# Kernel tuning notes

Measured on AMD Instinct MI355X. Metric: run time of the kernel, lower is better.

## Reference

```python
import jax, jax.numpy as jnp
import numpy as np

D_MODEL = 1024
EXPERT_SIZE = 512
N_EXPERTS = 8
GROUP_SIZE = 32
BATCH = 32
SEQ = 2048
TEMPERATURE = 1.0


def setup_inputs() -> dict:
    key = jax.random.key(0)
    k_x, k_l1, k_l2, k_c = jax.random.split(key, 4)
    x = jax.random.normal(k_x, (BATCH, SEQ, D_MODEL), dtype=jnp.float32)
    # truncated-normal-style init approximated with normal scaled by 1/sqrt(fan_in)
    lin1 = jax.random.normal(k_l1, (N_EXPERTS, D_MODEL, EXPERT_SIZE), dtype=jnp.float32) * (D_MODEL ** -0.5)
    lin2 = jax.random.normal(k_l2, (N_EXPERTS, EXPERT_SIZE, D_MODEL), dtype=jnp.float32) * (EXPERT_SIZE ** -0.5)
    controller = jax.random.normal(k_c, (D_MODEL, N_EXPERTS), dtype=jnp.float32) * (D_MODEL ** -0.5)
    return {"x": x, "lin1": lin1, "lin2": lin2, "controller": controller}


def reference(x, lin1, lin2, controller):
    B, S, D = x.shape
    # group_tokens: sparsity_dim=0 -> transpose to (S, B, D), split batch into groups
    xg = jnp.transpose(x, (1, 0, 2)).reshape(S, B // GROUP_SIZE, GROUP_SIZE, D)  # (s, g, k, d)
    # controller logits, softmax over the group (token) axis k (dim=-2)
    logits = jnp.einsum("sgkd,de->sgke", xg, controller) / TEMPERATURE
    merge_w = jax.nn.softmax(logits, axis=-2)  # (s, g, k, e)
    emit_w = merge_w  # default: emit softmax over tokens, same temp -> reuse
    # merge: weighted sum of tokens per expert
    merged = jnp.einsum("sgke,sgkd->sged", merge_w, xg)  # (s, g, e, d)
    # per-expert MLP
    h = jax.nn.relu(jnp.einsum("sged,edf->sgef", merged, lin1))  # (s, g, e, f)
    expert_out = jnp.einsum("sgef,efd->sged", h, lin2)  # (s, g, e, d)
    # emit back to tokens
    out = jnp.einsum("sgke,sged->sgkd", emit_w, expert_out)  # (s, g, k, d)
    # redistribute: (S, B, D) -> (B, S, D)
    return jnp.transpose(out.reshape(S, B, D), (1, 0, 2))
```

## Files before the change

### kernel.cpp

```cpp
#include <hip/hip_runtime.h>
#include <hip/hip_bf16.h>

#define SS 2048
#define BB 32
#define DD 1024
#define FF 512
#define EE 8

typedef __attribute__((ext_vector_type(8))) short short8;
typedef __attribute__((ext_vector_type(8))) unsigned short ushort8v;
typedef __attribute__((ext_vector_type(4))) float f32x4;

__device__ inline unsigned short f2bf(float f) {
  union { float f; unsigned u; } v; v.f = f;
  return (unsigned short)((v.u + 0x7FFFu + ((v.u >> 16) & 1u)) >> 16);
}
__device__ inline float bf2f(unsigned short h) {
  union { unsigned u; float f; } v; v.u = ((unsigned)h) << 16;
  return v.f;
}

__global__ __launch_bounds__(256) void transpose_bf16(
    const float* __restrict__ in, unsigned short* __restrict__ out, int K, int N) {
  __shared__ float tile[32][33];
  int e = blockIdx.z;
  const float* inp = in + (size_t)e * K * N;
  unsigned short* outp = out + (size_t)e * K * N;
  int k0 = blockIdx.x * 32, n0 = blockIdx.y * 32;
  int tx = threadIdx.x;
  int ty = threadIdx.y;
#pragma unroll
  for (int i = 0; i < 4; i++) {
    int k = ty + i * 8;
    tile[k][tx] = inp[(size_t)(k0 + k) * N + n0 + tx];
  }
  __syncthreads();
#pragma unroll
  for (int i = 0; i < 4; i++) {
    int n = ty + i * 8;
    outp[(size_t)(n0 + n) * K + k0 + tx] = f2bf(tile[tx][n]);
  }
}

__global__ __launch_bounds__(256) void ctrl_merge(
    const float* __restrict__ x,
    const float* __restrict__ ctrl,
    unsigned short* __restrict__ merged,
    float* __restrict__ mw) {
  int s = blockIdx.x;
  int t = threadIdx.x;
  __shared__ float cs[DD * EE];
  __shared__ float lg[BB][EE];
  for (int i = t; i < DD * EE; i += 256) cs[i] = ctrl[i];
  __syncthreads();

  int k = t >> 3, e = t & 7;
  const float* xr = x + ((size_t)k * SS + s) * DD;
  float acc = 0.f;
  for (int d = 0; d < DD; d += 4) {
    float4 xv = *(const float4*)&xr[d];
    acc += xv.x * cs[d * 8 + e] + xv.y * cs[(d + 1) * 8 + e] +
           xv.z * cs[(d + 2) * 8 + e] + xv.w * cs[(d + 3) * 8 + e];
  }
  lg[k][e] = acc;
  __syncthreads();

  if (t < EE) {
    float m = -1e30f;
    for (int kk = 0; kk < BB; kk++) m = fmaxf(m, lg[kk][t]);
    float sum = 0.f;
    for (int kk = 0; kk < BB; kk++) sum += __expf(lg[kk][t] - m);
    float inv = 1.f / sum;
    for (int kk = 0; kk < BB; kk++) {
      float w = __expf(lg[kk][t] - m) * inv;
      lg[kk][t] = w;
      mw[((size_t)s * BB + kk) * EE + t] = w;
    }
  }
  __syncthreads();

  float accm[EE][4];
#pragma unroll
  for (int ee = 0; ee < EE; ee++)
#pragma unroll
    for (int j = 0; j < 4; j++) accm[ee][j] = 0.f;
  for (int kk = 0; kk < BB; kk++) {
    float w0 = lg[kk][0], w1 = lg[kk][1], w2 = lg[kk][2], w3 = lg[kk][3];
    float w4 = lg[kk][4], w5 = lg[kk][5], w6 = lg[kk][6], w7 = lg[kk][7];
#pragma unroll
    for (int j = 0; j < 4; j++) {
      float xv = x[((size_t)kk * SS + s) * DD + j * 256 + t];
      accm[0][j] += w0 * xv; accm[1][j] += w1 * xv;
      accm[2][j] += w2 * xv; accm[3][j] += w3 * xv;
      accm[4][j] += w4 * xv; accm[5][j] += w5 * xv;
      accm[6][j] += w6 * xv; accm[7][j] += w7 * xv;
    }
  }
#pragma unroll
  for (int ee = 0; ee < EE; ee++)
#pragma unroll
    for (int j = 0; j < 4; j++)
      merged[((size_t)s * EE + ee) * DD + j * 256 + t] = f2bf(accm[ee][j]);
}

template <int RELU>
__global__ __launch_bounds__(256) void gemm_bt(
    const unsigned short* __restrict__ A, const unsigned short* __restrict__ Bt,
    unsigned short* __restrict__ C, int K, int N) {
  int e = blockIdx.z;
  int m0 = blockIdx.x * 128;
  int n0 = blockIdx.y * 128;
  const int lda = EE * K;
  const unsigned short* Ae = A + (size_t)e * K;
  const unsigned short* Be = Bt + (size_t)e * N * K;

  __shared__ __align__(16) unsigned short As[128][40];
  __shared__ __align__(16) unsigned short Bs[128][40];

  int t = threadIdx.x;
  int lane = t & 63, w = t >> 6;
  int wm = w >> 1, wn = w & 1;
  int lr = lane & 15;
  int kh = lane >> 4;

  f32x4 acc[4][4] = {};

  for (int kt = 0; kt < K; kt += 32) {
#pragma unroll
    for (int i = 0; i < 2; i++) {
      int o = t + i * 256;
      int r = o >> 2, c8 = (o & 3) * 8;
      ushort8v va = *(const ushort8v*)&Ae[(size_t)(m0 + r) * lda + kt + c8];
      *(ushort8v*)&As[r][c8] = va;
      ushort8v vb = *(const ushort8v*)&Be[(size_t)(n0 + r) * K + kt + c8];
      *(ushort8v*)&Bs[r][c8] = vb;
    }
    __syncthreads();

    short8 af[4], bfr[4];
#pragma unroll
    for (int mi = 0; mi < 4; mi++)
      af[mi] = *(const short8*)&As[wm * 64 + mi * 16 + lr][kh * 8];
#pragma unroll
    for (int ni = 0; ni < 4; ni++)
      bfr[ni] = *(const short8*)&Bs[wn * 64 + ni * 16 + lr][kh * 8];
#pragma unroll
    for (int mi = 0; mi < 4; mi++)
#pragma unroll
      for (int ni = 0; ni < 4; ni++)
        acc[mi][ni] = __builtin_amdgcn_mfma_f32_16x16x32_bf16(af[mi], bfr[ni], acc[mi][ni], 0, 0, 0);
    __syncthreads();
  }

  int rb = (lane >> 4) * 4;
  int cb = lane & 15;
#pragma unroll
  for (int mi = 0; mi < 4; mi++)
#pragma unroll
    for (int ni = 0; ni < 4; ni++)
#pragma unroll
      for (int r = 0; r < 4; r++) {
        float v = acc[mi][ni][r];
        if (RELU) v = fmaxf(v, 0.f);
        int m = m0 + wm * 64 + mi * 16 + rb + r;
        int n = n0 + wn * 64 + ni * 16 + cb;
        C[(size_t)m * (EE * N) + (size_t)e * N + n] = f2bf(v);
      }
}

__global__ __launch_bounds__(256) void emit_out(
    const unsigned short* __restrict__ eo,
    const float* __restrict__ mw,
    float* __restrict__ out) {
  int s = blockIdx.x;
  int t = threadIdx.x;
  __shared__ float w[BB][EE];
  w[t >> 3][t & 7] = mw[(size_t)s * BB * EE + t];
  __syncthreads();
  float ev[EE][4];
#pragma unroll
  for (int ee = 0; ee < EE; ee++)
#pragma unroll
    for (int j = 0; j < 4; j++)
      ev[ee][j] = bf2f(eo[((size_t)s * EE + ee) * DD + j * 256 + t]);
  for (int b = 0; b < BB; b++) {
#pragma unroll
    for (int j = 0; j < 4; j++) {
      float acc = 0.f;
#pragma unroll
      for (int ee = 0; ee < EE; ee++) acc += w[b][ee] * ev[ee][j];
      out[((size_t)b * SS + s) * DD + j * 256 + t] = acc;
    }
  }
}

extern "C" void kernel_launch(void* const* d_in, const int* in_sizes, int n_in,
                              void* d_out, int out_size, void* d_ws, size_t ws_size,
                              hipStream_t stream) {
  const float* x = (const float*)d_in[0];
  const float* lin1 = (const float*)d_in[1];
  const float* lin2 = (const float*)d_in[2];
  const float* ctrl = (const float*)d_in[3];
  float* out = (float*)d_out;

  char* ws = (char*)d_ws;
  size_t off = 0;
  unsigned short* lin1t = (unsigned short*)(ws + off); off += (size_t)EE * DD * FF * 2;
  unsigned short* lin2t = (unsigned short*)(ws + off); off += (size_t)EE * FF * DD * 2;
  unsigned short* merged = (unsigned short*)(ws + off); off += (size_t)SS * EE * DD * 2;
  unsigned short* hbuf = (unsigned short*)(ws + off); off += (size_t)SS * EE * FF * 2;
  unsigned short* eo = (unsigned short*)(ws + off); off += (size_t)SS * EE * DD * 2;
  float* mw = (float*)(ws + off); off += (size_t)SS * BB * EE * 4;

  dim3 tb(32, 8);
  transpose_bf16<<<dim3(DD / 32, FF / 32, EE), tb, 0, stream>>>(lin1, lin1t, DD, FF);
  transpose_bf16<<<dim3(FF / 32, DD / 32, EE), tb, 0, stream>>>(lin2, lin2t, FF, DD);

  ctrl_merge<<<SS, 256, 0, stream>>>(x, ctrl, merged, mw);

  gemm_bt<1><<<dim3(SS / 128, FF / 128, EE), 256, 0, stream>>>(merged, lin1t, hbuf, DD, FF);
  gemm_bt<0><<<dim3(SS / 128, DD / 128, EE), 256, 0, stream>>>(hbuf, lin2t, eo, FF, DD);

  emit_out<<<SS, 256, 0, stream>>>(eo, mw, out);
}
```

Measured before the change: 317.4 us.

## Restructure controller-merge kernel with LDS-staged x and coalesced vector I/O

Rewrites ctrl_merge to use 512 threads and read each x row once with coalesced float4 loads. It stages a bf16 copy of the 32 tokens in LDS for the merge pass instead of rereading x from global memory. Logits are reduced with wave shuffles, and the softmax runs in parallel across lanes. emit_out switches to 4-wide bf16 loads and float4 stores. The cost is bf16 rounding of x before the merge, a small accuracy change, plus about 80KB of LDS per block, which limits occupancy.

```diff
diff --git a/kernel.cpp b/kernel.cpp
--- a/kernel.cpp
+++ b/kernel.cpp
@@ -9,6 +9,7 @@
 
 typedef __attribute__((ext_vector_type(8))) short short8;
 typedef __attribute__((ext_vector_type(8))) unsigned short ushort8v;
+typedef __attribute__((ext_vector_type(4))) unsigned short ushort4v;
 typedef __attribute__((ext_vector_type(4))) float f32x4;
 
 __device__ inline unsigned short f2bf(float f) {
@@ -42,65 +43,110 @@
   }
 }
 
-__global__ __launch_bounds__(256) void ctrl_merge(
+__global__ __launch_bounds__(512) void ctrl_merge(
     const float* __restrict__ x,
     const float* __restrict__ ctrl,
     unsigned short* __restrict__ merged,
     float* __restrict__ mw) {
   int s = blockIdx.x;
   int t = threadIdx.x;
-  __shared__ float cs[DD * EE];
-  __shared__ float lg[BB][EE];
-  for (int i = t; i < DD * EE; i += 256) cs[i] = ctrl[i];
-  __syncthreads();
-
-  int k = t >> 3, e = t & 7;
-  const float* xr = x + ((size_t)k * SS + s) * DD;
-  float acc = 0.f;
-  for (int d = 0; d < DD; d += 4) {
-    float4 xv = *(const float4*)&xr[d];
-    acc += xv.x * cs[d * 8 + e] + xv.y * cs[(d + 1) * 8 + e] +
-           xv.z * cs[(d + 2) * 8 + e] + xv.w * cs[(d + 3) * 8 + e];
-  }
-  lg[k][e] = acc;
-  __syncthreads();
-
-  if (t < EE) {
-    float m = -1e30f;
-    for (int kk = 0; kk < BB; kk++) m = fmaxf(m, lg[kk][t]);
-    float sum = 0.f;
-    for (int kk = 0; kk < BB; kk++) sum += __expf(lg[kk][t] - m);
-    float inv = 1.f / sum;
-    for (int kk = 0; kk < BB; kk++) {
-      float w = __expf(lg[kk][t] - m) * inv;
-      lg[kk][t] = w;
-      mw[((size_t)s * BB + kk) * EE + t] = w;
+  int lane = t & 63, w = t >> 6;
+
+  __shared__ float cs[EE][DD];
+  __shared__ unsigned short xs[BB][DD];
+  __shared__ float wl[BB][EE];
+
+  for (int i = t; i < DD * EE; i += 512) {
+    int e2 = i >> 10, d = i & 1023;
+    cs[e2][d] = ctrl[(size_t)d * EE + e2];
+  }
+  __syncthreads();
+
+  float acc[4][8] = {};
+#pragma unroll
+  for (int i = 0; i < 4; i++) {
+    int dbase = lane * 4 + i * 256;
+    float4 c4[8];
+#pragma unroll
+    for (int e2 = 0; e2 < 8; e2++) c4[e2] = *(const float4*)&cs[e2][dbase];
+#pragma unroll
+    for (int kk = 0; kk < 4; kk++) {
+      int k = (w << 2) + kk;
+      float4 xv = *(const float4*)&x[((size_t)k * SS + s) * DD + dbase];
+      ushort4v pv;
+      pv[0] = f2bf(xv.x); pv[1] = f2bf(xv.y); pv[2] = f2bf(xv.z); pv[3] = f2bf(xv.w);
+      *(ushort4v*)&xs[k][dbase] = pv;
+#pragma unroll
+      for (int e2 = 0; e2 < 8; e2++)
+        acc[kk][e2] += xv.x * c4[e2].x + xv.y * c4[e2].y + xv.z * c4[e2].z + xv.w * c4[e2].w;
     }
   }
-  __syncthreads();
-
-  float accm[EE][4];
-#pragma unroll
-  for (int ee = 0; ee < EE; ee++)
-#pragma unroll
-    for (int j = 0; j < 4; j++) accm[ee][j] = 0.f;
-  for (int kk = 0; kk < BB; kk++) {
-    float w0 = lg[kk][0], w1 = lg[kk][1], w2 = lg[kk][2], w3 = lg[kk][3];
-    float w4 = lg[kk][4], w5 = lg[kk][5], w6 = lg[kk][6], w7 = lg[kk][7];
-#pragma unroll
-    for (int j = 0; j < 4; j++) {
-      float xv = x[((size_t)kk * SS + s) * DD + j * 256 + t];
-      accm[0][j] += w0 * xv; accm[1][j] += w1 * xv;
-      accm[2][j] += w2 * xv; accm[3][j] += w3 * xv;
-      accm[4][j] += w4 * xv; accm[5][j] += w5 * xv;
-      accm[6][j] += w6 * xv; accm[7][j] += w7 * xv;
-    }
-  }
-#pragma unroll
-  for (int ee = 0; ee < EE; ee++)
-#pragma unroll
-    for (int j = 0; j < 4; j++)
-      merged[((size_t)s * EE + ee) * DD + j * 256 + t] = f2bf(accm[ee][j]);
+#pragma unroll
+  for (int off = 1; off < 64; off <<= 1)
+#pragma unroll
+    for (int kk = 0; kk < 4; kk++)
+#pragma unroll
+      for (int e2 = 0; e2 < 8; e2++)
+        acc[kk][e2] += __shfl_xor(acc[kk][e2], off, 64);
+  if (lane == 0) {
+#pragma unroll
+    for (int kk = 0; kk < 4; kk++)
+#pragma unroll
+      for (int e2 = 0; e2 < 8; e2++)
+        wl[(w << 2) + kk][e2] = acc[kk][e2];
+  }
+  __syncthreads();
+
+  if (t < 32) {
+    float lgv[8], mx[8], p[8], sm[8];
+#pragma unroll
+    for (int e2 = 0; e2 < 8; e2++) { lgv[e2] = wl[t][e2]; mx[e2] = lgv[e2]; }
+#pragma unroll
+    for (int off = 1; off < 32; off <<= 1)
+#pragma unroll
+      for (int e2 = 0; e2 < 8; e2++)
+        mx[e2] = fmaxf(mx[e2], __shfl_xor(mx[e2], off, 64));
+#pragma unroll
+    for (int e2 = 0; e2 < 8; e2++) { p[e2] = __expf(lgv[e2] - mx[e2]); sm[e2] = p[e2]; }
+#pragma unroll
+    for (int off = 1; off < 32; off <<= 1)
+#pragma unroll
+      for (int e2 = 0; e2 < 8; e2++)
+        sm[e2] += __shfl_xor(sm[e2], off, 64);
+    float wv[8];
+#pragma unroll
+    for (int e2 = 0; e2 < 8; e2++) { wv[e2] = p[e2] / sm[e2]; wl[t][e2] = wv[e2]; }
+    float4 mv0 = {wv[0], wv[1], wv[2], wv[3]};
+    float4 mv1 = {wv[4], wv[5], wv[6], wv[7]};
+    float* mwp = &mw[((size_t)s * BB + t) * EE];
+    *(float4*)mwp = mv0;
+    *(float4*)(mwp + 4) = mv1;
+  }
+  __syncthreads();
+
+  int d0 = t << 1;
+  float a0[8] = {}, a1[8] = {};
+#pragma unroll 4
+  for (int k = 0; k < 32; k++) {
+    unsigned xv = *(const unsigned*)&xs[k][d0];
+    float x0 = bf2f((unsigned short)xv);
+    float x1 = bf2f((unsigned short)(xv >> 16));
+    float4 wA = *(const float4*)&wl[k][0];
+    float4 wB = *(const float4*)&wl[k][4];
+    a0[0] += wA.x * x0; a1[0] += wA.x * x1;
+    a0[1] += wA.y * x0; a1[1] += wA.y * x1;
+    a0[2] += wA.z * x0; a1[2] += wA.z * x1;
+    a0[3] += wA.w * x0; a1[3] += wA.w * x1;
+    a0[4] += wB.x * x0; a1[4] += wB.x * x1;
+    a0[5] += wB.y * x0; a1[5] += wB.y * x1;
+    a0[6] += wB.z * x0; a1[6] += wB.z * x1;
+    a0[7] += wB.w * x0; a1[7] += wB.w * x1;
+  }
+#pragma unroll
+  for (int e2 = 0; e2 < 8; e2++) {
+    unsigned pm = (unsigned)f2bf(a0[e2]) | ((unsigned)f2bf(a1[e2]) << 16);
+    *(unsigned*)&merged[((size_t)s * EE + e2) * DD + d0] = pm;
+  }
 }
 
 template <int RELU>
@@ -174,23 +220,27 @@
     float* __restrict__ out) {
   int s = blockIdx.x;
   int t = threadIdx.x;
-  __shared__ float w[BB][EE];
-  w[t >> 3][t & 7] = mw[(size_t)s * BB * EE + t];
-  __syncthreads();
+  __shared__ float wsm[BB][EE];
+  wsm[t >> 3][t & 7] = mw[(size_t)s * BB * EE + t];
+  __syncthreads();
+  int d0 = t * 4;
   float ev[EE][4];
 #pragma unroll
-  for (int ee = 0; ee < EE; ee++)
-#pragma unroll
-    for (int j = 0; j < 4; j++)
-      ev[ee][j] = bf2f(eo[((size_t)s * EE + ee) * DD + j * 256 + t]);
+  for (int e2 = 0; e2 < 8; e2++) {
+    ushort4v v = *(const ushort4v*)&eo[((size_t)s * EE + e2) * DD + d0];
+    ev[e2][0] = bf2f(v[0]); ev[e2][1] = bf2f(v[1]);
+    ev[e2][2] = bf2f(v[2]); ev[e2][3] = bf2f(v[3]);
+  }
   for (int b = 0; b < BB; b++) {
-#pragma unroll
-    for (int j = 0; j < 4; j++) {
-      float acc = 0.f;
-#pragma unroll
-      for (int ee = 0; ee < EE; ee++) acc += w[b][ee] * ev[ee][j];
-      out[((size_t)b * SS + s) * DD + j * 256 + t] = acc;
+    float o0 = 0.f, o1 = 0.f, o2 = 0.f, o3 = 0.f;
+#pragma unroll
+    for (int e2 = 0; e2 < 8; e2++) {
+      float we = wsm[b][e2];
+      o0 += we * ev[e2][0]; o1 += we * ev[e2][1];
+      o2 += we * ev[e2][2]; o3 += we * ev[e2][3];
     }
+    float4 ov = {o0, o1, o2, o3};
+    *(float4*)&out[((size_t)b * SS + s) * DD + d0] = ov;
   }
 }
 
@@ -216,7 +266,7 @@
   transpose_bf16<<<dim3(DD / 32, FF / 32, EE), tb, 0, stream>>>(lin1, lin1t, DD, FF);
   transpose_bf16<<<dim3(FF / 32, DD / 32, EE), tb, 0, stream>>>(lin2, lin2t, FF, DD);
 
-  ctrl_merge<<<SS, 256, 0, stream>>>(x, ctrl, merged, mw);
+  ctrl_merge<<<SS, 512, 0, stream>>>(x, ctrl, merged, mw);
 
   gemm_bt<1><<<dim3(SS / 128, FF / 128, EE), 256, 0, stream>>>(merged, lin1t, hbuf, DD, FF);
   gemm_bt<0><<<dim3(SS / 128, DD / 128, EE), 256, 0, stream>>>(hbuf, lin2t, eo, FF, DD);
```

New measurement: 328.0 us. +3.3%, slower.
